# Kernel tuning notes

Measured on AMD Instinct MI355X. Metric: run time of the kernel, lower is better.

The kernel has to match this reference:

```python
import jax, jax.numpy as jnp
import numpy as np

EMB_DIM = 1024
NUM_HEADS = 16
SCALE_WEIGHTS = 1.0
TINY = jnp.finfo(jnp.float32).tiny


def setup_inputs() -> dict:
    key = jax.random.key(0)
    k1, k2, k3 = jax.random.split(key, 3)
    B, S = 2, 2048
    x = jax.random.normal(k1, (B, S, EMB_DIM), dtype=jnp.float32)
    weights = jax.random.uniform(k2, (B, S), dtype=jnp.float32)
    W_qkv = jax.random.normal(k3, (EMB_DIM, 3 * EMB_DIM), dtype=jnp.float32) / np.sqrt(EMB_DIM)
    b_qkv = jnp.zeros((3 * EMB_DIM,), dtype=jnp.float32)
    return {"x": x, "weights": weights, "W_qkv": W_qkv, "b_qkv": b_qkv}


def reference(x, weights, W_qkv, b_qkv):
    B, S, E = x.shape
    H = NUM_HEADS
    hd = E // H
    # QKV projection: [B,S,3E] -> [B,H,S,3*hd] -> split
    qkv = x @ W_qkv + b_qkv
    qkv = qkv.reshape(B, S, H, 3 * hd).transpose(0, 2, 1, 3)
    q, k, v = jnp.split(qkv, 3, axis=-1)  # each [B,H,S,hd]
    # weights: [B,S] -> [B,1,1,S] (broadcast over heads and query positions)
    w = weights[:, None, None, :]
    # scores with log-weight bias and hard masks
    attn_logits = jnp.einsum("bhqd,bhkd->bhqk", q, k) / jnp.sqrt(jnp.asarray(hd, x.dtype))
    attn_logits = attn_logits + jnp.log(w / SCALE_WEIGHTS + TINY)
    attn_logits = jnp.where(w == 0, -9e15, attn_logits)
    attn_logits = jnp.where(w == 1, 9e15, attn_logits)
    attention = jax.nn.softmax(attn_logits, axis=-1)
    values = jnp.einsum("bhqk,bhkd->bhqd", attention, v)
    return values.transpose(0, 2, 1, 3).reshape(B, S, E)
```

## Files before the change

### kernel.cpp

```cpp
#include <hip/hip_runtime.h>
#include <math.h>

#define B_  2
#define S_  2048
#define E_  1024
#define H_  16
#define HD_ 64
#define N3_ 3072
#define M_  (B_*S_)

typedef _Float16 h8  __attribute__((ext_vector_type(8)));
typedef _Float16 h4  __attribute__((ext_vector_type(4)));
typedef float    f4  __attribute__((ext_vector_type(4)));
typedef float    fv16 __attribute__((ext_vector_type(16)));

typedef __attribute__((address_space(3))) unsigned int       lds_u32;
typedef const __attribute__((address_space(1))) unsigned int glob_u32;

__device__ __forceinline__ void gld16(const void* g, void* l) {
    __builtin_amdgcn_global_load_lds((glob_u32*)g, (lds_u32*)l, 16, 0, 0);
}
__device__ __forceinline__ float exp2_hw(float x) { return __builtin_amdgcn_exp2f(x); }

#define QSCALE 0.18033688011112042f
#define RESCALE_THR 8.0f

__global__ void cvt_x_kernel(const float* __restrict__ x, _Float16* __restrict__ x16) {
    int i = (blockIdx.x * 256 + threadIdx.x) * 8;
    float4 u = *(const float4*)&x[i];
    float4 v = *(const float4*)&x[i + 4];
    h8 o;
    o[0] = (_Float16)u.x; o[1] = (_Float16)u.y; o[2] = (_Float16)u.z; o[3] = (_Float16)u.w;
    o[4] = (_Float16)v.x; o[5] = (_Float16)v.y; o[6] = (_Float16)v.z; o[7] = (_Float16)v.w;
    *(h8*)&x16[i] = o;
}

__global__ __launch_bounds__(256) void transpose_w_kernel(
        const float* __restrict__ W, _Float16* __restrict__ Wt) {
    __shared__ float T[64][65];
    int k0 = blockIdx.x * 64, n0 = blockIdx.y * 64;
    int tid = threadIdx.x;
    int r = tid >> 4, c4 = (tid & 15) * 4;
#pragma unroll
    for (int i = 0; i < 4; i++) {
        int row = r + i * 16;
        float4 u = *(const float4*)&W[(size_t)(k0 + row) * N3_ + n0 + c4];
        T[c4 + 0][row] = u.x; T[c4 + 1][row] = u.y;
        T[c4 + 2][row] = u.z; T[c4 + 3][row] = u.w;
    }
    __syncthreads();
#pragma unroll
    for (int i = 0; i < 4; i++) {
        int rn = r + i * 16;
        h4 p;
        p[0] = (_Float16)T[rn][c4 + 0]; p[1] = (_Float16)T[rn][c4 + 1];
        p[2] = (_Float16)T[rn][c4 + 2]; p[3] = (_Float16)T[rn][c4 + 3];
        *(h4*)&Wt[(size_t)(n0 + rn) * E_ + k0 + c4] = p;
    }
}

__global__ __launch_bounds__(256, 2) void qkv_gemm32(
        const _Float16* __restrict__ x16, const _Float16* __restrict__ wt,
        const float* __restrict__ bq, const float* __restrict__ w,
        _Float16* __restrict__ qws, _Float16* __restrict__ kws,
        _Float16* __restrict__ vtws) {
    __shared__ __align__(16) _Float16 Ab[2][128 * 64];
    __shared__ __align__(16) _Float16 Wb[2][192 * 64];

    int tid = threadIdx.x;
    int wid = tid >> 6, lane = tid & 63;
    int l31 = lane & 31, hi = lane >> 5, l7 = l31 & 7;
    int srow = lane >> 3;
    int wm = wid & 1, wn = wid >> 1;

    int L = blockIdx.x;
    int head = 2 * (L & 7) + (L >> 8);
    int mb = (L >> 3) & 31;
    int m0 = mb * 128;
    int n0 = head * 192;
    int b = m0 >> 11;
    int bh = b * H_ + head;
    int sblk = m0 & 2047;

    fv16 acc[2][3];
#pragma unroll
    for (int ntl = 0; ntl < 3; ntl++) {
        int n_abs = wn * 96 + ntl * 32;
        int which = n_abs >> 6;
        fv16 ini;
        if (which == 2) {
            float bb = bq[n0 + n_abs + l31];
#pragma unroll
            for (int r = 0; r < 16; r++) ini[r] = bb;
        } else {
#pragma unroll
            for (int g = 0; g < 4; g++) {
                f4 bv = *(const f4*)&bq[n0 + n_abs + 8 * g + 4 * hi];
#pragma unroll
                for (int j = 0; j < 4; j++) ini[4 * g + j] = bv[j];
            }
        }
        acc[0][ntl] = ini; acc[1][ntl] = ini;
    }

    auto stage = [&](int t, int bf) {
        int k0 = t * 64;
#pragma unroll
        for (int j = 0; j < 4; j++) {
            int batch = wid * 4 + j;
            int row = batch * 8 + srow;
            int ch = (lane & 7) ^ srow ^ (batch & 7);
            gld16(&x16[(size_t)(m0 + row) * E_ + k0 + ch * 8], &Ab[bf][batch * 8 * 64]);
        }
#pragma unroll
        for (int j = 0; j < 6; j++) {
            int batch = wid * 6 + j;
            int row = batch * 8 + srow;
            int ch = (lane & 7) ^ srow ^ (batch & 7);
            gld16(&wt[(size_t)(n0 + row) * E_ + k0 + ch * 8], &Wb[bf][batch * 8 * 64]);
        }
    };

    stage(0, 0);

    for (int t = 0; t < 16; t++) {
        int bf = t & 1;
        __syncthreads();
        if (t < 15) stage(t + 1, bf ^ 1);
#pragma unroll
        for (int step = 0; step < 4; step++) {
            h8 af[2], wf[3];
#pragma unroll
            for (int mt = 0; mt < 2; mt++) {
                int R = wm * 64 + mt * 32 + l31;
                int ph = ((2 * step + hi) ^ l7 ^ ((mt * 4 + (l31 >> 3)) & 7)) * 8;
                af[mt] = *(const h8*)&Ab[bf][R * 64 + ph];
            }
#pragma unroll
            for (int ntl = 0; ntl < 3; ntl++) {
                int R = wn * 96 + ntl * 32 + l31;
                int ph = ((2 * step + hi) ^ l7 ^ ((wn * 12 + ntl * 4 + (l31 >> 3)) & 7)) * 8;
                wf[ntl] = *(const h8*)&Wb[bf][R * 64 + ph];
            }
#pragma unroll
            for (int ntl = 0; ntl < 3; ntl++) {
                bool isv = (wn == 1) && (ntl >= 1);
#pragma unroll
                for (int mt = 0; mt < 2; mt++) {
                    if (isv)
                        acc[mt][ntl] = __builtin_amdgcn_mfma_f32_32x32x16_f16(af[mt], wf[ntl], acc[mt][ntl], 0, 0, 0);
                    else
                        acc[mt][ntl] = __builtin_amdgcn_mfma_f32_32x32x16_f16(wf[ntl], af[mt], acc[mt][ntl], 0, 0, 0);
                }
            }
        }
    }

#pragma unroll
    for (int ntl = 0; ntl < 3; ntl++) {
        int n_abs = wn * 96 + ntl * 32;
        int which = n_abs >> 6;
#pragma unroll
        for (int mt = 0; mt < 2; mt++) {
            if (which == 2) {
                int d = (n_abs & 63) + l31;
#pragma unroll
                for (int g = 0; g < 4; g++) {
                    int soff = wm * 64 + mt * 32 + 8 * g + 4 * hi;
                    f4 wf4 = *(const f4*)&w[m0 + soff];
                    h4 p;
#pragma unroll
                    for (int j = 0; j < 4; j++)
                        p[j] = (_Float16)(acc[mt][ntl][4 * g + j] * wf4[j]);
                    *(h4*)&vtws[((size_t)bh * 64 + d) * S_ + sblk + soff] = p;
                }
            } else {
                _Float16* dst = (which == 0) ? qws : kws;
                float scale = (which == 0) ? QSCALE : 1.0f;
                int s = sblk + wm * 64 + mt * 32 + l31;
#pragma unroll
                for (int g = 0; g < 4; g++) {
                    int d0 = (n_abs & 63) + 8 * g + 4 * hi;
                    h4 p;
#pragma unroll
                    for (int j = 0; j < 4; j++)
                        p[j] = (_Float16)(acc[mt][ntl][4 * g + j] * scale);
                    *(h4*)&dst[((size_t)bh * S_ + s) * 64 + d0] = p;
                }
            }
        }
    }
}

__global__ __launch_bounds__(256, 2) void attn_kernel(
        const _Float16* __restrict__ q, const _Float16* __restrict__ k,
        const _Float16* __restrict__ vt, const float* __restrict__ w,
        float* __restrict__ out) {
    __shared__ __align__(16) _Float16 Kb[2][64 * 64];
    __shared__ __align__(16) _Float16 Vb[2][64 * 64];
    __shared__ __align__(16) float lws[2048];

    int tid = threadIdx.x;
    int wid = tid >> 6, lane = tid & 63;
    int l31 = lane & 31, hi = lane >> 5, l7 = l31 & 7;
    int srow = lane >> 3;
    int L = blockIdx.x;
    int bh = (L & 7) + 8 * (L >> 7);
    int qt = (L >> 3) & 15;
    int q0 = qt * 128;
    int b = bh >> 4, h = bh & 15;

    const _Float16* qbase = q + (size_t)bh * S_ * HD_;
    const _Float16* kbase = k + (size_t)bh * S_ * HD_;
    const _Float16* vbase = vt + (size_t)bh * HD_ * S_;
    const float* wbase = w + (size_t)b * S_;

#pragma unroll
    for (int j = 0; j < 2; j++) {
        int batch = wid + 4 * j;
        gld16(&wbase[batch * 256 + lane * 4], &lws[batch * 256]);
    }

    auto stage = [&](int kt, int bf) {
        int k0 = kt * 64;
#pragma unroll
        for (int j = 0; j < 2; j++) {
            int batch = wid * 2 + j;
            int row = batch * 8 + srow;
            int ch = (lane & 7) ^ srow ^ (batch & 7);
            gld16(&kbase[(size_t)(k0 + row) * 64 + ch * 8], &Kb[bf][batch * 8 * 64]);
            gld16(&vbase[(size_t)row * S_ + k0 + ch * 8], &Vb[bf][batch * 8 * 64]);
        }
    };

    stage(0, 0);

    int qrow = q0 + wid * 32 + l31;
    h8 qf[4];
#pragma unroll
    for (int step = 0; step < 4; step++)
        qf[step] = *(const h8*)&qbase[(size_t)qrow * 64 + 16 * step + 8 * hi];

    fv16 o[2];
    o[0] = (fv16)0.0f; o[1] = (fv16)0.0f;
    float m_r = -INFINITY, l_r = 0.0f;

    for (int kt = 0; kt < 32; kt++) {
        int bf = kt & 1;
        __syncthreads();
        if (kt < 31) stage(kt + 1, bf ^ 1);

        fv16 st[2];
        st[0] = (fv16)0.0f; st[1] = (fv16)0.0f;
        __builtin_amdgcn_s_setprio(1);
#pragma unroll
        for (int step = 0; step < 4; step++) {
#pragma unroll
            for (int kt2 = 0; kt2 < 2; kt2++) {
                int R = kt2 * 32 + l31;
                int ph = ((2 * step + hi) ^ l7 ^ ((kt2 * 4 + (l31 >> 3)) & 7)) * 8;
                h8 kf = *(const h8*)&Kb[bf][R * 64 + ph];
                st[kt2] = __builtin_amdgcn_mfma_f32_32x32x16_f16(kf, qf[step], st[kt2], 0, 0, 0);
            }
        }
        __builtin_amdgcn_s_setprio(0);

        float tm[16];
#pragma unroll
        for (int r = 0; r < 16; r++) tm[r] = fmaxf(st[0][r], st[1][r]);
#pragma unroll
        for (int r = 0; r < 8; r++) tm[r] = fmaxf(tm[r], tm[r + 8]);
#pragma unroll
        for (int r = 0; r < 4; r++) tm[r] = fmaxf(tm[r], tm[r + 4]);
        float pmax = fmaxf(fmaxf(tm[0], tm[1]), fmaxf(tm[2], tm[3]));

        if (!__all(pmax <= m_r + RESCALE_THR)) {
            float rowmax = fmaxf(pmax, __shfl_xor(pmax, 32));
            float mnew = fmaxf(m_r, rowmax);
            float alpha = exp2_hw(m_r - mnew);
            m_r = mnew;
            l_r *= alpha;
            o[0] = o[0] * alpha;
            o[1] = o[1] * alpha;
        }

        f4 rsv = (f4)0.0f;
        h4 pf[2][4];
        int k0 = kt * 64;
#pragma unroll
        for (int kt2 = 0; kt2 < 2; kt2++)
#pragma unroll
            for (int g = 0; g < 4; g++) {
                f4 wv = *(const f4*)&lws[k0 + kt2 * 32 + 8 * g + 4 * hi];
                f4 e;
#pragma unroll
                for (int j = 0; j < 4; j++) {
                    float ev = exp2_hw(st[kt2][4 * g + j] - m_r);
                    e[j] = ev;
                    rsv[j] += ev * wv[j];
                }
                h4 p;
                p[0] = (_Float16)e[0]; p[1] = (_Float16)e[1];
                p[2] = (_Float16)e[2]; p[3] = (_Float16)e[3];
                pf[kt2][g] = p;
            }
        l_r += (rsv[0] + rsv[1]) + (rsv[2] + rsv[3]);

        __builtin_amdgcn_s_setprio(1);
#pragma unroll
        for (int kt2 = 0; kt2 < 2; kt2++)
#pragma unroll
            for (int g = 0; g < 4; g++) {
                int c = 4 * kt2 + g;
#pragma unroll
                for (int dt = 0; dt < 2; dt++) {
                    int R = dt * 32 + l31;
                    int ph = (c ^ l7 ^ ((dt * 4 + (l31 >> 3)) & 7)) * 8 + hi * 4;
                    h4 vf = *(const h4*)&Vb[bf][R * 64 + ph];
                    o[dt] = __builtin_amdgcn_mfma_f32_32x32x8f16(vf, pf[kt2][g], o[dt], 0, 0, 0);
                }
            }
        __builtin_amdgcn_s_setprio(0);
    }

    float lsum = l_r + __shfl_xor(l_r, 32);
    float linv = 1.0f / lsum;
    float* obase = &out[((size_t)(b * S_ + qrow)) * E_ + h * 64];
#pragma unroll
    for (int dt = 0; dt < 2; dt++)
#pragma unroll
        for (int g = 0; g < 4; g++) {
            int d0 = dt * 32 + 8 * g + 4 * hi;
            f4 ov;
#pragma unroll
            for (int j = 0; j < 4; j++) ov[j] = o[dt][4 * g + j] * linv;
            *(f4*)&obase[d0] = ov;
        }
}

extern "C" void kernel_launch(void* const* d_in, const int* in_sizes, int n_in,
                              void* d_out, int out_size, void* d_ws, size_t ws_size,
                              hipStream_t stream) {
    const float* x  = (const float*)d_in[0];
    const float* w  = (const float*)d_in[1];
    const float* Wq = (const float*)d_in[2];
    const float* bq = (const float*)d_in[3];
    float* out = (float*)d_out;

    char* p = (char*)d_ws;
    _Float16* x16 = (_Float16*)p;              p += (size_t)M_ * E_ * 2;
    _Float16* wt  = (_Float16*)p;              p += (size_t)E_ * N3_ * 2;
    _Float16* qb  = (_Float16*)p;              p += (size_t)M_ * E_ * 2;
    _Float16* kb  = (_Float16*)p;              p += (size_t)M_ * E_ * 2;
    _Float16* vtb = (_Float16*)p;

    cvt_x_kernel<<<dim3(M_ * E_ / 2048), dim3(256), 0, stream>>>(x, x16);
    transpose_w_kernel<<<dim3(E_ / 64, N3_ / 64), dim3(256), 0, stream>>>(Wq, wt);
    qkv_gemm32<<<dim3(512), dim3(256), 0, stream>>>(x16, wt, bq, w, qb, kb, vtb);
    attn_kernel<<<dim3(512), dim3(256), 0, stream>>>(qb, kb, vtb, w, out);
}
```

Baseline: 178.5 us.

## Widen attention key tile to 128 and merge prep conversion kernels

The attention kernel now stages 128 keys per iteration as two 64-key halves in a double buffer. This halves the number of barriers and the online-softmax max/rescale checks per query tile, but doubles LDS use for K/V and holds more score accumulators in registers. Separately, the x-to-fp16 conversion and the weight transpose are fused into one launch to save a kernel launch. Occupancy may drop under the two-block launch bound.

```diff
diff --git a/kernel.cpp b/kernel.cpp
--- a/kernel.cpp
+++ b/kernel.cpp
@@ -25,37 +25,40 @@
 #define QSCALE 0.18033688011112042f
 #define RESCALE_THR 8.0f
 
-__global__ void cvt_x_kernel(const float* __restrict__ x, _Float16* __restrict__ x16) {
-    int i = (blockIdx.x * 256 + threadIdx.x) * 8;
-    float4 u = *(const float4*)&x[i];
-    float4 v = *(const float4*)&x[i + 4];
-    h8 o;
-    o[0] = (_Float16)u.x; o[1] = (_Float16)u.y; o[2] = (_Float16)u.z; o[3] = (_Float16)u.w;
-    o[4] = (_Float16)v.x; o[5] = (_Float16)v.y; o[6] = (_Float16)v.z; o[7] = (_Float16)v.w;
-    *(h8*)&x16[i] = o;
-}
-
-__global__ __launch_bounds__(256) void transpose_w_kernel(
+__global__ __launch_bounds__(256) void prep_kernel(
+        const float* __restrict__ x, _Float16* __restrict__ x16,
         const float* __restrict__ W, _Float16* __restrict__ Wt) {
     __shared__ float T[64][65];
-    int k0 = blockIdx.x * 64, n0 = blockIdx.y * 64;
+    int L = blockIdx.x;
     int tid = threadIdx.x;
-    int r = tid >> 4, c4 = (tid & 15) * 4;
-#pragma unroll
-    for (int i = 0; i < 4; i++) {
-        int row = r + i * 16;
-        float4 u = *(const float4*)&W[(size_t)(k0 + row) * N3_ + n0 + c4];
-        T[c4 + 0][row] = u.x; T[c4 + 1][row] = u.y;
-        T[c4 + 2][row] = u.z; T[c4 + 3][row] = u.w;
-    }
-    __syncthreads();
-#pragma unroll
-    for (int i = 0; i < 4; i++) {
-        int rn = r + i * 16;
-        h4 p;
-        p[0] = (_Float16)T[rn][c4 + 0]; p[1] = (_Float16)T[rn][c4 + 1];
-        p[2] = (_Float16)T[rn][c4 + 2]; p[3] = (_Float16)T[rn][c4 + 3];
-        *(h4*)&Wt[(size_t)(n0 + rn) * E_ + k0 + c4] = p;
+    if (L < 2048) {
+        int i = (L * 256 + tid) * 8;
+        float4 u = *(const float4*)&x[i];
+        float4 v = *(const float4*)&x[i + 4];
+        h8 o;
+        o[0] = (_Float16)u.x; o[1] = (_Float16)u.y; o[2] = (_Float16)u.z; o[3] = (_Float16)u.w;
+        o[4] = (_Float16)v.x; o[5] = (_Float16)v.y; o[6] = (_Float16)v.z; o[7] = (_Float16)v.w;
+        *(h8*)&x16[i] = o;
+    } else {
+        int L2 = L - 2048;
+        int k0 = (L2 & 15) * 64, n0 = (L2 >> 4) * 64;
+        int r = tid >> 4, c4 = (tid & 15) * 4;
+#pragma unroll
+        for (int i = 0; i < 4; i++) {
+            int row = r + i * 16;
+            float4 u = *(const float4*)&W[(size_t)(k0 + row) * N3_ + n0 + c4];
+            T[c4 + 0][row] = u.x; T[c4 + 1][row] = u.y;
+            T[c4 + 2][row] = u.z; T[c4 + 3][row] = u.w;
+        }
+        __syncthreads();
+#pragma unroll
+        for (int i = 0; i < 4; i++) {
+            int rn = r + i * 16;
+            h4 p;
+            p[0] = (_Float16)T[rn][c4 + 0]; p[1] = (_Float16)T[rn][c4 + 1];
+            p[2] = (_Float16)T[rn][c4 + 2]; p[3] = (_Float16)T[rn][c4 + 3];
+            *(h4*)&Wt[(size_t)(n0 + rn) * E_ + k0 + c4] = p;
+        }
     }
 }
 
@@ -196,8 +199,8 @@
         const _Float16* __restrict__ q, const _Float16* __restrict__ k,
         const _Float16* __restrict__ vt, const float* __restrict__ w,
         float* __restrict__ out) {
-    __shared__ __align__(16) _Float16 Kb[2][64 * 64];
-    __shared__ __align__(16) _Float16 Vb[2][64 * 64];
+    __shared__ __align__(16) _Float16 Kb[2][2][64 * 64];
+    __shared__ __align__(16) _Float16 Vb[2][2][64 * 64];
     __shared__ __align__(16) float lws[2048];
 
     int tid = threadIdx.x;
@@ -221,15 +224,18 @@
         gld16(&wbase[batch * 256 + lane * 4], &lws[batch * 256]);
     }
 
-    auto stage = [&](int kt, int bf) {
-        int k0 = kt * 64;
-#pragma unroll
-        for (int j = 0; j < 2; j++) {
-            int batch = wid * 2 + j;
-            int row = batch * 8 + srow;
-            int ch = (lane & 7) ^ srow ^ (batch & 7);
-            gld16(&kbase[(size_t)(k0 + row) * 64 + ch * 8], &Kb[bf][batch * 8 * 64]);
-            gld16(&vbase[(size_t)row * S_ + k0 + ch * 8], &Vb[bf][batch * 8 * 64]);
+    auto stage = [&](int t, int bf) {
+#pragma unroll
+        for (int half = 0; half < 2; half++) {
+            int k0 = t * 128 + half * 64;
+#pragma unroll
+            for (int j = 0; j < 2; j++) {
+                int batch = wid * 2 + j;
+                int row = batch * 8 + srow;
+                int ch = l7 ^ srow ^ (batch & 7);
+                gld16(&kbase[(size_t)(k0 + row) * 64 + ch * 8], &Kb[bf][half][batch * 8 * 64]);
+                gld16(&vbase[(size_t)row * S_ + k0 + ch * 8], &Vb[bf][half][batch * 8 * 64]);
+            }
         }
     };
 
@@ -245,29 +251,33 @@
     o[0] = (fv16)0.0f; o[1] = (fv16)0.0f;
     float m_r = -INFINITY, l_r = 0.0f;
 
-    for (int kt = 0; kt < 32; kt++) {
-        int bf = kt & 1;
+    for (int t = 0; t < 16; t++) {
+        int bf = t & 1;
         __syncthreads();
-        if (kt < 31) stage(kt + 1, bf ^ 1);
-
-        fv16 st[2];
-        st[0] = (fv16)0.0f; st[1] = (fv16)0.0f;
+        if (t < 15) stage(t + 1, bf ^ 1);
+
+        fv16 st[2][2];
+        st[0][0] = (fv16)0.0f; st[0][1] = (fv16)0.0f;
+        st[1][0] = (fv16)0.0f; st[1][1] = (fv16)0.0f;
         __builtin_amdgcn_s_setprio(1);
 #pragma unroll
-        for (int step = 0; step < 4; step++) {
-#pragma unroll
-            for (int kt2 = 0; kt2 < 2; kt2++) {
-                int R = kt2 * 32 + l31;
-                int ph = ((2 * step + hi) ^ l7 ^ ((kt2 * 4 + (l31 >> 3)) & 7)) * 8;
-                h8 kf = *(const h8*)&Kb[bf][R * 64 + ph];
-                st[kt2] = __builtin_amdgcn_mfma_f32_32x32x16_f16(kf, qf[step], st[kt2], 0, 0, 0);
-            }
-        }
+        for (int half = 0; half < 2; half++)
+#pragma unroll
+            for (int step = 0; step < 4; step++)
+#pragma unroll
+                for (int kt2 = 0; kt2 < 2; kt2++) {
+                    int R = kt2 * 32 + l31;
+                    int ph = ((2 * step + hi) ^ l7 ^ ((kt2 * 4 + (l31 >> 3)) & 7)) * 8;
+                    h8 kf = *(const h8*)&Kb[bf][half][R * 64 + ph];
+                    st[half][kt2] = __builtin_amdgcn_mfma_f32_32x32x16_f16(kf, qf[step], st[half][kt2], 0, 0, 0);
+                }
         __builtin_amdgcn_s_setprio(0);
 
         float tm[16];
 #pragma unroll
-        for (int r = 0; r < 16; r++) tm[r] = fmaxf(st[0][r], st[1][r]);
+        for (int r = 0; r < 16; r++)
+            tm[r] = fmaxf(fmaxf(st[0][0][r], st[0][1][r]),
+                          fmaxf(st[1][0][r], st[1][1][r]));
 #pragma unroll
         for (int r = 0; r < 8; r++) tm[r] = fmaxf(tm[r], tm[r + 8]);
 #pragma unroll
@@ -284,43 +294,46 @@
             o[1] = o[1] * alpha;
         }
 
-        f4 rsv = (f4)0.0f;
-        h4 pf[2][4];
-        int k0 = kt * 64;
-#pragma unroll
-        for (int kt2 = 0; kt2 < 2; kt2++)
-#pragma unroll
-            for (int g = 0; g < 4; g++) {
-                f4 wv = *(const f4*)&lws[k0 + kt2 * 32 + 8 * g + 4 * hi];
-                f4 e;
-#pragma unroll
-                for (int j = 0; j < 4; j++) {
-                    float ev = exp2_hw(st[kt2][4 * g + j] - m_r);
-                    e[j] = ev;
-                    rsv[j] += ev * wv[j];
-                }
-                h4 p;
-                p[0] = (_Float16)e[0]; p[1] = (_Float16)e[1];
-                p[2] = (_Float16)e[2]; p[3] = (_Float16)e[3];
-                pf[kt2][g] = p;
-            }
-        l_r += (rsv[0] + rsv[1]) + (rsv[2] + rsv[3]);
-
-        __builtin_amdgcn_s_setprio(1);
-#pragma unroll
-        for (int kt2 = 0; kt2 < 2; kt2++)
-#pragma unroll
-            for (int g = 0; g < 4; g++) {
-                int c = 4 * kt2 + g;
-#pragma unroll
-                for (int dt = 0; dt < 2; dt++) {
-                    int R = dt * 32 + l31;
-                    int ph = (c ^ l7 ^ ((dt * 4 + (l31 >> 3)) & 7)) * 8 + hi * 4;
-                    h4 vf = *(const h4*)&Vb[bf][R * 64 + ph];
-                    o[dt] = __builtin_amdgcn_mfma_f32_32x32x8f16(vf, pf[kt2][g], o[dt], 0, 0, 0);
-                }
-            }
-        __builtin_amdgcn_s_setprio(0);
+#pragma unroll
+        for (int half = 0; half < 2; half++) {
+            int k0 = t * 128 + half * 64;
+            f4 rsv = (f4)0.0f;
+            h4 pf[2][4];
+#pragma unroll
+            for (int kt2 = 0; kt2 < 2; kt2++)
+#pragma unroll
+                for (int g = 0; g < 4; g++) {
+                    f4 wv = *(const f4*)&lws[k0 + kt2 * 32 + 8 * g + 4 * hi];
+                    f4 e;
+#pragma unroll
+                    for (int j = 0; j < 4; j++) {
+                        float ev = exp2_hw(st[half][kt2][4 * g + j] - m_r);
+                        e[j] = ev;
+                        rsv[j] += ev * wv[j];
+                    }
+                    h4 p;
+                    p[0] = (_Float16)e[0]; p[1] = (_Float16)e[1];
+                    p[2] = (_Float16)e[2]; p[3] = (_Float16)e[3];
+                    pf[kt2][g] = p;
+                }
+            l_r += (rsv[0] + rsv[1]) + (rsv[2] + rsv[3]);
+
+            __builtin_amdgcn_s_setprio(1);
+#pragma unroll
+            for (int kt2 = 0; kt2 < 2; kt2++)
+#pragma unroll
+                for (int g = 0; g < 4; g++) {
+                    int c = 4 * kt2 + g;
+#pragma unroll
+                    for (int dt = 0; dt < 2; dt++) {
+                        int R = dt * 32 + l31;
+                        int ph = (c ^ l7 ^ ((dt * 4 + (l31 >> 3)) & 7)) * 8 + hi * 4;
+                        h4 vf = *(const h4*)&Vb[bf][half][R * 64 + ph];
+                        o[dt] = __builtin_amdgcn_mfma_f32_32x32x8f16(vf, pf[kt2][g], o[dt], 0, 0, 0);
+                    }
+                }
+            __builtin_amdgcn_s_setprio(0);
+        }
     }
 
     float lsum = l_r + __shfl_xor(l_r, 32);
@@ -354,8 +367,7 @@
     _Float16* kb  = (_Float16*)p;              p += (size_t)M_ * E_ * 2;
     _Float16* vtb = (_Float16*)p;
 
-    cvt_x_kernel<<<dim3(M_ * E_ / 2048), dim3(256), 0, stream>>>(x, x16);
-    transpose_w_kernel<<<dim3(E_ / 64, N3_ / 64), dim3(256), 0, stream>>>(Wq, wt);
+    prep_kernel<<<dim3(2048 + 768), dim3(256), 0, stream>>>(x, x16, Wq, wt);
     qkv_gemm32<<<dim3(512), dim3(256), 0, stream>>>(x16, wt, bq, w, qb, kb, vtb);
     attn_kernel<<<dim3(512), dim3(256), 0, stream>>>(qb, kb, vtb, w, out);
 }
```

New measurement: 180.1 us. No clear change (+0.9%).

## Compute weighted softmax denominator via MFMA and merge prep kernels

Applied to the files above, without the earlier changes.

Converts the per-key weights to fp16 and computes the weighted row sum of exponentials with an extra MFMA against a weight vector, instead of scalar FMA accumulation in the inner loop. The x conversion, weight conversion and W transpose are merged into a single prep kernel, saving a launch. The row max reduction now uses three-input max, and exponentials are packed to fp16 with cvt_pkrtz. In exchange, the denominator picks up fp16 rounding of both the weights and the exponentials, and each tile issues more MFMA work.

```diff
diff --git a/kernel.cpp b/kernel.cpp
--- a/kernel.cpp
+++ b/kernel.cpp
@@ -11,6 +11,8 @@
 
 typedef _Float16 h8  __attribute__((ext_vector_type(8)));
 typedef _Float16 h4  __attribute__((ext_vector_type(4)));
+typedef _Float16 h2  __attribute__((ext_vector_type(2)));
+typedef __fp16   fp16x2 __attribute__((ext_vector_type(2)));
 typedef float    f4  __attribute__((ext_vector_type(4)));
 typedef float    fv16 __attribute__((ext_vector_type(16)));
 
@@ -21,41 +23,54 @@
     __builtin_amdgcn_global_load_lds((glob_u32*)g, (lds_u32*)l, 16, 0, 0);
 }
 __device__ __forceinline__ float exp2_hw(float x) { return __builtin_amdgcn_exp2f(x); }
+__device__ __forceinline__ float fmax3(float a, float b, float c) {
+    return fmaxf(fmaxf(a, b), c);
+}
+__device__ __forceinline__ h2 cvt_pk_f16(float a, float b) {
+    fp16x2 r = __builtin_amdgcn_cvt_pkrtz(a, b);
+    return __builtin_bit_cast(h2, r);
+}
 
 #define QSCALE 0.18033688011112042f
 #define RESCALE_THR 8.0f
 
-__global__ void cvt_x_kernel(const float* __restrict__ x, _Float16* __restrict__ x16) {
-    int i = (blockIdx.x * 256 + threadIdx.x) * 8;
-    float4 u = *(const float4*)&x[i];
-    float4 v = *(const float4*)&x[i + 4];
-    h8 o;
-    o[0] = (_Float16)u.x; o[1] = (_Float16)u.y; o[2] = (_Float16)u.z; o[3] = (_Float16)u.w;
-    o[4] = (_Float16)v.x; o[5] = (_Float16)v.y; o[6] = (_Float16)v.z; o[7] = (_Float16)v.w;
-    *(h8*)&x16[i] = o;
-}
-
-__global__ __launch_bounds__(256) void transpose_w_kernel(
+__global__ __launch_bounds__(256) void prep_kernel(
+        const float* __restrict__ x, _Float16* __restrict__ x16,
+        const float* __restrict__ w, _Float16* __restrict__ w16,
         const float* __restrict__ W, _Float16* __restrict__ Wt) {
     __shared__ float T[64][65];
-    int k0 = blockIdx.x * 64, n0 = blockIdx.y * 64;
+    int L = blockIdx.x;
     int tid = threadIdx.x;
-    int r = tid >> 4, c4 = (tid & 15) * 4;
-#pragma unroll
-    for (int i = 0; i < 4; i++) {
-        int row = r + i * 16;
-        float4 u = *(const float4*)&W[(size_t)(k0 + row) * N3_ + n0 + c4];
-        T[c4 + 0][row] = u.x; T[c4 + 1][row] = u.y;
-        T[c4 + 2][row] = u.z; T[c4 + 3][row] = u.w;
-    }
-    __syncthreads();
-#pragma unroll
-    for (int i = 0; i < 4; i++) {
-        int rn = r + i * 16;
-        h4 p;
-        p[0] = (_Float16)T[rn][c4 + 0]; p[1] = (_Float16)T[rn][c4 + 1];
-        p[2] = (_Float16)T[rn][c4 + 2]; p[3] = (_Float16)T[rn][c4 + 3];
-        *(h4*)&Wt[(size_t)(n0 + rn) * E_ + k0 + c4] = p;
+    if (L < 2050) {
+        const float* src = (L < 2048) ? &x[(size_t)L * 2048] : &w[(size_t)(L - 2048) * 2048];
+        _Float16* dst    = (L < 2048) ? &x16[(size_t)L * 2048] : &w16[(size_t)(L - 2048) * 2048];
+        int i = tid * 8;
+        float4 u = *(const float4*)&src[i];
+        float4 v = *(const float4*)&src[i + 4];
+        h8 o;
+        o[0] = (_Float16)u.x; o[1] = (_Float16)u.y; o[2] = (_Float16)u.z; o[3] = (_Float16)u.w;
+        o[4] = (_Float16)v.x; o[5] = (_Float16)v.y; o[6] = (_Float16)v.z; o[7] = (_Float16)v.w;
+        *(h8*)&dst[i] = o;
+    } else {
+        int L2 = L - 2050;
+        int k0 = (L2 & 15) * 64, n0 = (L2 >> 4) * 64;
+        int r = tid >> 4, c4 = (tid & 15) * 4;
+#pragma unroll
+        for (int i = 0; i < 4; i++) {
+            int row = r + i * 16;
+            float4 u = *(const float4*)&W[(size_t)(k0 + row) * N3_ + n0 + c4];
+            T[c4 + 0][row] = u.x; T[c4 + 1][row] = u.y;
+            T[c4 + 2][row] = u.z; T[c4 + 3][row] = u.w;
+        }
+        __syncthreads();
+#pragma unroll
+        for (int i = 0; i < 4; i++) {
+            int rn = r + i * 16;
+            h4 p;
+            p[0] = (_Float16)T[rn][c4 + 0]; p[1] = (_Float16)T[rn][c4 + 1];
+            p[2] = (_Float16)T[rn][c4 + 2]; p[3] = (_Float16)T[rn][c4 + 3];
+            *(h4*)&Wt[(size_t)(n0 + rn) * E_ + k0 + c4] = p;
+        }
     }
 }
 
@@ -194,11 +209,11 @@
 
 __global__ __launch_bounds__(256, 2) void attn_kernel(
         const _Float16* __restrict__ q, const _Float16* __restrict__ k,
-        const _Float16* __restrict__ vt, const float* __restrict__ w,
+        const _Float16* __restrict__ vt, const _Float16* __restrict__ w16,
         float* __restrict__ out) {
     __shared__ __align__(16) _Float16 Kb[2][64 * 64];
     __shared__ __align__(16) _Float16 Vb[2][64 * 64];
-    __shared__ __align__(16) float lws[2048];
+    __shared__ __align__(16) _Float16 lws16[2048];
 
     int tid = threadIdx.x;
     int wid = tid >> 6, lane = tid & 63;
@@ -213,13 +228,9 @@
     const _Float16* qbase = q + (size_t)bh * S_ * HD_;
     const _Float16* kbase = k + (size_t)bh * S_ * HD_;
     const _Float16* vbase = vt + (size_t)bh * HD_ * S_;
-    const float* wbase = w + (size_t)b * S_;
-
-#pragma unroll
-    for (int j = 0; j < 2; j++) {
-        int batch = wid + 4 * j;
-        gld16(&wbase[batch * 256 + lane * 4], &lws[batch * 256]);
-    }
+    const _Float16* wbase = w16 + (size_t)b * S_;
+
+    gld16(&wbase[wid * 512 + lane * 8], &lws16[wid * 512]);
 
     auto stage = [&](int kt, int bf) {
         int k0 = kt * 64;
@@ -241,9 +252,9 @@
     for (int step = 0; step < 4; step++)
         qf[step] = *(const h8*)&qbase[(size_t)qrow * 64 + 16 * step + 8 * hi];
 
-    fv16 o[2];
-    o[0] = (fv16)0.0f; o[1] = (fv16)0.0f;
-    float m_r = -INFINITY, l_r = 0.0f;
+    fv16 o[2], ol;
+    o[0] = (fv16)0.0f; o[1] = (fv16)0.0f; ol = (fv16)0.0f;
+    float m_r = -INFINITY;
 
     for (int kt = 0; kt < 32; kt++) {
         int bf = kt & 1;
@@ -265,47 +276,45 @@
         }
         __builtin_amdgcn_s_setprio(0);
 
-        float tm[16];
-#pragma unroll
-        for (int r = 0; r < 16; r++) tm[r] = fmaxf(st[0][r], st[1][r]);
-#pragma unroll
-        for (int r = 0; r < 8; r++) tm[r] = fmaxf(tm[r], tm[r + 8]);
-#pragma unroll
-        for (int r = 0; r < 4; r++) tm[r] = fmaxf(tm[r], tm[r + 4]);
-        float pmax = fmaxf(fmaxf(tm[0], tm[1]), fmaxf(tm[2], tm[3]));
+        float tm[11];
+#pragma unroll
+        for (int r = 0; r < 10; r++)
+            tm[r] = fmax3(st[(3*r)>>4][(3*r)&15], st[(3*r+1)>>4][(3*r+1)&15],
+                          st[(3*r+2)>>4][(3*r+2)&15]);
+        tm[10] = fmaxf(st[1][14], st[1][15]);
+        float u0 = fmax3(tm[0], tm[1], tm[2]);
+        float u1 = fmax3(tm[3], tm[4], tm[5]);
+        float u2 = fmax3(tm[6], tm[7], tm[8]);
+        float u3 = fmaxf(tm[9], tm[10]);
+        float pmax = fmaxf(fmax3(u0, u1, u2), u3);
 
         if (!__all(pmax <= m_r + RESCALE_THR)) {
             float rowmax = fmaxf(pmax, __shfl_xor(pmax, 32));
             float mnew = fmaxf(m_r, rowmax);
             float alpha = exp2_hw(m_r - mnew);
             m_r = mnew;
-            l_r *= alpha;
             o[0] = o[0] * alpha;
             o[1] = o[1] * alpha;
-        }
-
-        f4 rsv = (f4)0.0f;
+            ol = ol * alpha;
+        }
+
         h4 pf[2][4];
+#pragma unroll
+        for (int kt2 = 0; kt2 < 2; kt2++)
+#pragma unroll
+            for (int g = 0; g < 4; g++) {
+                float e0 = exp2_hw(st[kt2][4 * g + 0] - m_r);
+                float e1 = exp2_hw(st[kt2][4 * g + 1] - m_r);
+                float e2 = exp2_hw(st[kt2][4 * g + 2] - m_r);
+                float e3 = exp2_hw(st[kt2][4 * g + 3] - m_r);
+                h2 p01 = cvt_pk_f16(e0, e1);
+                h2 p23 = cvt_pk_f16(e2, e3);
+                h4 p;
+                p[0] = p01[0]; p[1] = p01[1]; p[2] = p23[0]; p[3] = p23[1];
+                pf[kt2][g] = p;
+            }
+
         int k0 = kt * 64;
-#pragma unroll
-        for (int kt2 = 0; kt2 < 2; kt2++)
-#pragma unroll
-            for (int g = 0; g < 4; g++) {
-                f4 wv = *(const f4*)&lws[k0 + kt2 * 32 + 8 * g + 4 * hi];
-                f4 e;
-#pragma unroll
-                for (int j = 0; j < 4; j++) {
-                    float ev = exp2_hw(st[kt2][4 * g + j] - m_r);
-                    e[j] = ev;
-                    rsv[j] += ev * wv[j];
-                }
-                h4 p;
-                p[0] = (_Float16)e[0]; p[1] = (_Float16)e[1];
-                p[2] = (_Float16)e[2]; p[3] = (_Float16)e[3];
-                pf[kt2][g] = p;
-            }
-        l_r += (rsv[0] + rsv[1]) + (rsv[2] + rsv[3]);
-
         __builtin_amdgcn_s_setprio(1);
 #pragma unroll
         for (int kt2 = 0; kt2 < 2; kt2++)
@@ -319,12 +328,13 @@
                     h4 vf = *(const h4*)&Vb[bf][R * 64 + ph];
                     o[dt] = __builtin_amdgcn_mfma_f32_32x32x8f16(vf, pf[kt2][g], o[dt], 0, 0, 0);
                 }
+                h4 wf_ = *(const h4*)&lws16[k0 + c * 8 + 4 * hi];
+                ol = __builtin_amdgcn_mfma_f32_32x32x8f16(wf_, pf[kt2][g], ol, 0, 0, 0);
             }
         __builtin_amdgcn_s_setprio(0);
     }
 
-    float lsum = l_r + __shfl_xor(l_r, 32);
-    float linv = 1.0f / lsum;
+    float linv = 1.0f / ol[0];
     float* obase = &out[((size_t)(b * S_ + qrow)) * E_ + h * 64];
 #pragma unroll
     for (int dt = 0; dt < 2; dt++)
@@ -352,10 +362,10 @@
     _Float16* wt  = (_Float16*)p;              p += (size_t)E_ * N3_ * 2;
     _Float16* qb  = (_Float16*)p;              p += (size_t)M_ * E_ * 2;
     _Float16* kb  = (_Float16*)p;              p += (size_t)M_ * E_ * 2;
-    _Float16* vtb = (_Float16*)p;
-
-    cvt_x_kernel<<<dim3(M_ * E_ / 2048), dim3(256), 0, stream>>>(x, x16);
-    transpose_w_kernel<<<dim3(E_ / 64, N3_ / 64), dim3(256), 0, stream>>>(Wq, wt);
+    _Float16* vtb = (_Float16*)p;              p += (size_t)M_ * HD_ * H_ * 2;
+    _Float16* w16 = (_Float16*)p;
+
+    prep_kernel<<<dim3(2050 + 768), dim3(256), 0, stream>>>(x, x16, w, w16, Wq, wt);
     qkv_gemm32<<<dim3(512), dim3(256), 0, stream>>>(x16, wt, bq, w, qb, kb, vtb);
-    attn_kernel<<<dim3(512), dim3(256), 0, stream>>>(qb, kb, vtb, w, out);
-}
+    attn_kernel<<<dim3(512), dim3(256), 0, stream>>>(qb, kb, vtb, w16, out);
+}
```

Result: no change. 178.9 us (+0.2%).
